# Kernel optimization log

Hardware: AMD Instinct MI355X
Metric: run time of the kernel (lower is better)

## Reference

```python
import jax, jax.numpy as jnp
import numpy as np

B, T, CH, Hs, Ws = 2, 64, 512, 24, 24
DIM = CH // 2          # 256, attention channel dim
HEADS = 8
HEAD_DIM = DIM // HEADS  # 32
MAX_SEQ = 64


def setup_inputs() -> dict:
    key = jax.random.key(0)
    ks = jax.random.split(key, 6)
    return {
        "x": jax.random.normal(ks[0], (B, T, CH, Hs, Ws), dtype=jnp.float32),
        "rpb_table": jax.random.normal(ks[1], (2 * MAX_SEQ - 1, HEADS), dtype=jnp.float32) * 0.02,
        "qkv_w": jax.random.normal(ks[2], (3 * DIM, DIM), dtype=jnp.float32) * 0.02,
        "qkv_b": jax.random.normal(ks[3], (3 * DIM,), dtype=jnp.float32) * 0.02,
        "proj_w": jax.random.normal(ks[4], (DIM, DIM), dtype=jnp.float32) * 0.02,
        "proj_b": jax.random.normal(ks[5], (DIM,), dtype=jnp.float32) * 0.02,
    }


def reference(x, rpb_table, qkv_w, qkv_b, proj_w, proj_b):
    b, t, c, h, w = x.shape
    half = c // 2
    a_part = x[:, :, :half]       # (B,T,half,H,W) untouched branch
    b_part = x[:, :, half:]       # attention branch

    # 'b t c h w -> (b h w) t c'
    xb = jnp.transpose(b_part, (0, 3, 4, 1, 2)).reshape(b * h * w, t, half)
    B_, N, C = xb.shape
    scale = HEAD_DIM ** -0.5

    qkv = xb @ qkv_w.T + qkv_b                        # (B_, N, 3*C)
    qkv = qkv.reshape(B_, N, 3, HEADS, HEAD_DIM)
    qkv = jnp.transpose(qkv, (2, 0, 3, 1, 4))          # (3, B_, heads, N, hd)
    q, k, v = qkv[0] * scale, qkv[1], qkv[2]

    attn = jnp.einsum('bhnd,bhmd->bhnm', q, k)         # (B_, heads, N, N)

    # relative position bias: index = p2 - p1 + (MAX_SEQ - 1)
    pos = jnp.arange(t)
    rel_idx = pos[None, :] - pos[:, None] + (MAX_SEQ - 1)   # (N, N)
    bias = rpb_table[rel_idx]                              # (N, N, heads)
    bias = jnp.transpose(bias, (2, 0, 1))                  # (heads, N, N)
    attn = attn + bias[None]

    # causal (mask_future=True): -inf strictly above the diagonal
    causal = jnp.where(pos[None, :] > pos[:, None], -jnp.inf, 0.0).astype(attn.dtype)
    attn = attn + causal[None, None]

    attn = jax.nn.softmax(attn, axis=-1)

    out = jnp.einsum('bhnm,bhmd->bhnd', attn, v)       # (B_, heads, N, hd)
    out = jnp.transpose(out, (0, 2, 1, 3)).reshape(B_, N, C)
    out = out @ proj_w.T + proj_b

    # '(b h w) t c -> b t c h w'
    out = out.reshape(b, h, w, t, half)
    out = jnp.transpose(out, (0, 3, 4, 1, 2))

    return jnp.concatenate([a_part, out], axis=2)
```

## Files before the change

### kernel.cpp

```cpp
#include <hip/hip_runtime.h>
#include <hip/hip_bf16.h>

typedef __attribute__((ext_vector_type(4))) float  f32x4;
typedef __attribute__((ext_vector_type(8))) short  bf16x8;
typedef __attribute__((ext_vector_type(8))) unsigned short u16x8;

union FU { int w[4]; bf16x8 v; };

__device__ __forceinline__ unsigned short f2bf(float f) {
    union { float f; unsigned u; } v; v.f = f;
    unsigned u = v.u;
    unsigned r = u + 0x7fffu + ((u >> 16) & 1u);
    return (unsigned short)(r >> 16);
}

__device__ __forceinline__ unsigned cvtpk(float lo, float hi) {
    unsigned r;
    asm("v_cvt_pk_bf16_f32 %0, %1, %2" : "=v"(r) : "v"(lo), "v"(hi));
    return r;
}

__device__ __forceinline__ int selshfl(unsigned lo, unsigned hiw, int srcLane, bool hi) {
    int a = __shfl((int)lo, srcLane, 64);
    int b = __shfl((int)hiw, srcLane, 64);
    return hi ? b : a;
}

__device__ __forceinline__ void gload16(const void* g, void* l) {
    __builtin_amdgcn_global_load_lds((const __attribute__((address_space(1))) unsigned*)g,
                                     (__attribute__((address_space(3))) unsigned*)l, 16, 0, 0);
}


__global__ void cvt_weights(const float* __restrict__ qkv_w, const float* __restrict__ proj_w,
                            unsigned short* __restrict__ wq, unsigned short* __restrict__ wp) {
    int i = blockIdx.x * 256 + threadIdx.x;
    if (i < 196608) wq[i] = f2bf(qkv_w[i]);
    else            wp[i - 196608] = f2bf(proj_w[i - 196608]);
}

__global__ __launch_bounds__(256) void transpose_b(const float* __restrict__ x,
                                                   unsigned short* __restrict__ xb,
                                                   float* __restrict__ outp) {
    __shared__ unsigned short tile[256][72];
    const int bt  = blockIdx.x;
    const int hw0 = blockIdx.y * 64;
    const int tid = threadIdx.x;
    {
        const size_t slab = (size_t)bt * 294912;
        #pragma unroll
        for (int it = 0; it < 16; ++it) {
            int idx = it * 256 + tid;
            int ch  = idx >> 4;
            int off = (idx & 15) * 4;
            size_t o = slab + (size_t)ch * 576 + hw0 + off;
            *(float4*)(outp + o) = *(const float4*)(x + o);
        }
    }
    const float* src = x + ((size_t)bt * 512 + 256) * 576 + hw0;
    const int c_sub = tid >> 4, l16 = tid & 15;
    #pragma unroll
    for (int it = 0; it < 16; ++it) {
        int cc = it * 16 + c_sub;
        const float4 v = *(const float4*)(src + (size_t)cc * 576 + l16 * 4);
        tile[cc][l16 * 4 + 0] = f2bf(v.x);
        tile[cc][l16 * 4 + 1] = f2bf(v.y);
        tile[cc][l16 * 4 + 2] = f2bf(v.z);
        tile[cc][l16 * 4 + 3] = f2bf(v.w);
    }
    __syncthreads();
    const int row = tid >> 2;
    const int cs  = (tid & 3) * 64;
    const int b = bt >> 6, t = bt & 63;
    size_t m = ((size_t)(b * 576 + hw0 + row)) * 64 + t;
    unsigned short* dst = xb + m * 256 + cs;
    #pragma unroll
    for (int q = 0; q < 8; ++q) {
        u16x8 v;
        #pragma unroll
        for (int u = 0; u < 8; ++u) v[u] = tile[cs + q * 8 + u][row];
        *(u16x8*)(dst + q * 8) = v;
    }
}

__global__ __launch_bounds__(512, 4)
void fused_block(
    const unsigned short* __restrict__ xb,
    const unsigned short* __restrict__ wqkv,
    const unsigned short* __restrict__ wproj,
    const float* __restrict__ qkv_b,
    const float* __restrict__ proj_b,
    const float* __restrict__ rpb,
    float* __restrict__ out)
{
    __shared__ unsigned short xs[16384];
    __shared__ unsigned short VtAll[256 * 88];
    __shared__ float bias_s[8][64];

    const int tid  = threadIdx.x;
    const int lane = tid & 63, w = tid >> 6;
    const int c = lane & 15, g = lane >> 4;
    const int c7 = c & 7;
    const bool hi = g >= 2;
    const int lA = c + 16 * ((2 * g) & 3);
    const int lB = c + 16 * ((2 * g + 1) & 3);
    const int bid = blockIdx.x;
    const int p  = (bid & 7) * 144 + (bid >> 3);
    const int b  = p / 576, hw = p % 576;

    const unsigned short* src = xb + (size_t)p * 16384;
    #pragma unroll
    for (int it = 0; it < 4; ++it) {
        int U = it * 512 + tid;
        int r = U >> 5, u = U & 31;
        gload16(src + r * 256 + ((u ^ (r & 7)) << 3), &xs[U << 3]);
    }
    bias_s[tid & 7][tid >> 3] = rpb[tid];
    __syncthreads();

    const float* bias_w = bias_s[w];

    {
        f32x4 acc[2][4] = {};
        #pragma unroll
        for (int ks = 0; ks < 8; ++ks) {
            bf16x8 bx[4], af[2];
            #pragma unroll
            for (int b2 = 0; b2 < 4; ++b2)
                bx[b2] = *(const bf16x8*)(&xs[(b2 * 16 + c) * 256 + (((ks * 4 + g) ^ c7) << 3)]);
            #pragma unroll
            for (int a2 = 0; a2 < 2; ++a2)
                af[a2] = *(const bf16x8*)(wqkv + (size_t)(512 + w * 32 + a2 * 16 + c) * 256 + ks * 32 + g * 8);
            #pragma unroll
            for (int a2 = 0; a2 < 2; ++a2)
                #pragma unroll
                for (int b2 = 0; b2 < 4; ++b2)
                    acc[a2][b2] = __builtin_amdgcn_mfma_f32_16x16x32_bf16(af[a2], bx[b2], acc[a2][b2], 0, 0, 0);
        }
        #pragma unroll
        for (int a2 = 0; a2 < 2; ++a2) {
            float4 bv = *(const float4*)(qkv_b + 512 + w * 32 + a2 * 16 + g * 4);
            #pragma unroll
            for (int b2 = 0; b2 < 4; ++b2) {
                int t = b2 * 16 + c;
                VtAll[(w * 32 + a2 * 16 + g * 4 + 0) * 88 + t] = f2bf(acc[a2][b2][0] + bv.x);
                VtAll[(w * 32 + a2 * 16 + g * 4 + 1) * 88 + t] = f2bf(acc[a2][b2][1] + bv.y);
                VtAll[(w * 32 + a2 * 16 + g * 4 + 2) * 88 + t] = f2bf(acc[a2][b2][2] + bv.z);
                VtAll[(w * 32 + a2 * 16 + g * 4 + 3) * 88 + t] = f2bf(acc[a2][b2][3] + bv.w);
            }
        }
    }

    unsigned kpk[2][4][2], qpk[2][4][2];
    {
        f32x4 ak[2][4] = {}, aq[2][4] = {};
        #pragma unroll
        for (int ks = 0; ks < 8; ++ks) {
            bf16x8 bx[4], afk[2], afq[2];
            #pragma unroll
            for (int b2 = 0; b2 < 4; ++b2)
                bx[b2] = *(const bf16x8*)(&xs[(b2 * 16 + c) * 256 + (((ks * 4 + g) ^ c7) << 3)]);
            #pragma unroll
            for (int a2 = 0; a2 < 2; ++a2) {
                afk[a2] = *(const bf16x8*)(wqkv + (size_t)(256 + w * 32 + a2 * 16 + c) * 256 + ks * 32 + g * 8);
                afq[a2] = *(const bf16x8*)(wqkv + (size_t)(      w * 32 + a2 * 16 + c) * 256 + ks * 32 + g * 8);
            }
            #pragma unroll
            for (int a2 = 0; a2 < 2; ++a2)
                #pragma unroll
                for (int b2 = 0; b2 < 4; ++b2) {
                    ak[a2][b2] = __builtin_amdgcn_mfma_f32_16x16x32_bf16(afk[a2], bx[b2], ak[a2][b2], 0, 0, 0);
                    aq[a2][b2] = __builtin_amdgcn_mfma_f32_16x16x32_bf16(afq[a2], bx[b2], aq[a2][b2], 0, 0, 0);
                }
        }
        #pragma unroll
        for (int a2 = 0; a2 < 2; ++a2) {
            float4 bk = *(const float4*)(qkv_b + 256 + w * 32 + a2 * 16 + g * 4);
            float4 bq = *(const float4*)(qkv_b +       w * 32 + a2 * 16 + g * 4);
            #pragma unroll
            for (int b2 = 0; b2 < 4; ++b2) {
                kpk[a2][b2][0] = cvtpk(ak[a2][b2][0] + bk.x, ak[a2][b2][1] + bk.y);
                kpk[a2][b2][1] = cvtpk(ak[a2][b2][2] + bk.z, ak[a2][b2][3] + bk.w);
                qpk[a2][b2][0] = cvtpk(aq[a2][b2][0] + bq.x, aq[a2][b2][1] + bq.y);
                qpk[a2][b2][1] = cvtpk(aq[a2][b2][2] + bq.z, aq[a2][b2][3] + bq.w);
            }
        }
    }

    bf16x8 kf[4], qf[4];
    #pragma unroll
    for (int t = 0; t < 4; ++t) {
        FU f;
        f.w[0] = selshfl(kpk[0][t][0], kpk[1][t][0], lA, hi);
        f.w[1] = selshfl(kpk[0][t][1], kpk[1][t][1], lA, hi);
        f.w[2] = selshfl(kpk[0][t][0], kpk[1][t][0], lB, hi);
        f.w[3] = selshfl(kpk[0][t][1], kpk[1][t][1], lB, hi);
        kf[t] = f.v;
        FU f2;
        f2.w[0] = selshfl(qpk[0][t][0], qpk[1][t][0], lA, hi);
        f2.w[1] = selshfl(qpk[0][t][1], qpk[1][t][1], lA, hi);
        f2.w[2] = selshfl(qpk[0][t][0], qpk[1][t][0], lB, hi);
        f2.w[3] = selshfl(qpk[0][t][1], qpk[1][t][1], lB, hi);
        qf[t] = f2.v;
    }
    f32x4 S[4][4];
    #pragma unroll
    for (int jt = 0; jt < 4; ++jt)
        #pragma unroll
        for (int it = 0; it < 4; ++it)
            S[jt][it] = f32x4{0.f, 0.f, 0.f, 0.f};
    __builtin_amdgcn_s_setprio(1);
    #pragma unroll
    for (int jt = 0; jt < 4; ++jt)
        #pragma unroll
        for (int it = 0; it < 4; ++it)
            S[jt][it] = __builtin_amdgcn_mfma_f32_16x16x32_bf16(kf[jt], qf[it], S[jt][it], 0, 0, 0);
    __builtin_amdgcn_s_setprio(0);

    const float scale = 0.17677669529663687f;
    unsigned ppk[4][4][2];
    #pragma unroll
    for (int it = 0; it < 4; ++it) {
        float rs = 0.f;
        #pragma unroll
        for (int jt = 0; jt < 4; ++jt)
            #pragma unroll
            for (int r = 0; r < 4; ++r) {
                int j = jt * 16 + 4 * g + r;
                int i = it * 16 + c;
                int d = j - i + 63; d = d > 63 ? 63 : d;
                float v = S[jt][it][r] * scale + bias_w[d];
                float e = (j > i) ? 0.f : __expf(v);
                S[jt][it][r] = e;
                rs += e;
            }
        rs += __shfl_xor(rs, 16, 64);
        rs += __shfl_xor(rs, 32, 64);
        float inv = 1.0f / rs;
        #pragma unroll
        for (int jt = 0; jt < 4; ++jt) {
            ppk[jt][it][0] = cvtpk(S[jt][it][0] * inv, S[jt][it][1] * inv);
            ppk[jt][it][1] = cvtpk(S[jt][it][2] * inv, S[jt][it][3] * inv);
        }
    }

    bf16x8 vf[2][2];
    #pragma unroll
    for (int dt = 0; dt < 2; ++dt)
        #pragma unroll
        for (int kk = 0; kk < 2; ++kk)
            vf[dt][kk] = *(const bf16x8*)(&VtAll[(w * 32 + dt * 16 + c) * 88 + kk * 32 + g * 8]);
    f32x4 O[2][4];
    #pragma unroll
    for (int dt = 0; dt < 2; ++dt)
        #pragma unroll
        for (int it = 0; it < 4; ++it)
            O[dt][it] = f32x4{0.f, 0.f, 0.f, 0.f};
    #pragma unroll
    for (int it = 0; it < 4; ++it) {
        #pragma unroll
        for (int kk = 0; kk < 2; ++kk) {
            FU pf;
            pf.w[0] = selshfl(ppk[2 * kk][it][0], ppk[2 * kk + 1][it][0], lA, hi);
            pf.w[1] = selshfl(ppk[2 * kk][it][1], ppk[2 * kk + 1][it][1], lA, hi);
            pf.w[2] = selshfl(ppk[2 * kk][it][0], ppk[2 * kk + 1][it][0], lB, hi);
            pf.w[3] = selshfl(ppk[2 * kk][it][1], ppk[2 * kk + 1][it][1], lB, hi);
            __builtin_amdgcn_s_setprio(1);
            #pragma unroll
            for (int dt = 0; dt < 2; ++dt)
                O[dt][it] = __builtin_amdgcn_mfma_f32_16x16x32_bf16(vf[dt][kk], pf.v, O[dt][it], 0, 0, 0);
            __builtin_amdgcn_s_setprio(0);
        }
    }

    __syncthreads();
    #pragma unroll
    for (int dt = 0; dt < 2; ++dt)
        #pragma unroll
        for (int it = 0; it < 4; ++it)
            #pragma unroll
            for (int r = 0; r < 4; ++r) {
                int t  = it * 16 + c;
                int cg = w * 32 + dt * 16 + 4 * g + r;
                xs[t * 256 + ((((cg >> 3) ^ (t & 7)) << 3) | (cg & 7))] = f2bf(O[dt][it][r]);
            }
    __syncthreads();

    f32x4 ap[2][4] = {};
    #pragma unroll
    for (int ks = 0; ks < 8; ++ks) {
        bf16x8 af[2], bx[4];
        #pragma unroll
        for (int a2 = 0; a2 < 2; ++a2)
            af[a2] = *(const bf16x8*)(wproj + (size_t)(w * 32 + a2 * 16 + c) * 256 + ks * 32 + g * 8);
        #pragma unroll
        for (int b2 = 0; b2 < 4; ++b2)
            bx[b2] = *(const bf16x8*)(&xs[(b2 * 16 + c) * 256 + (((ks * 4 + g) ^ c7) << 3)]);
        #pragma unroll
        for (int a2 = 0; a2 < 2; ++a2)
            #pragma unroll
            for (int b2 = 0; b2 < 4; ++b2)
                ap[a2][b2] = __builtin_amdgcn_mfma_f32_16x16x32_bf16(af[a2], bx[b2], ap[a2][b2], 0, 0, 0);
    }
    #pragma unroll
    for (int a2 = 0; a2 < 2; ++a2) {
        int n = w * 32 + a2 * 16 + g * 4;
        float4 pb = *(const float4*)(proj_b + n);
        #pragma unroll
        for (int b2 = 0; b2 < 4; ++b2) {
            int t = b2 * 16 + c;
            float* dst = out + ((size_t)((b * 64 + t) * 512 + 256 + n)) * 576 + hw;
            dst[0]        = ap[a2][b2][0] + pb.x;
            dst[576]      = ap[a2][b2][1] + pb.y;
            dst[2 * 576]  = ap[a2][b2][2] + pb.z;
            dst[3 * 576]  = ap[a2][b2][3] + pb.w;
        }
    }
}

extern "C" void kernel_launch(void* const* d_in, const int* in_sizes, int n_in,
                              void* d_out, int out_size, void* d_ws, size_t ws_size,
                              hipStream_t stream) {
    (void)in_sizes; (void)n_in; (void)out_size;
    const float* x      = (const float*)d_in[0];
    const float* rpb    = (const float*)d_in[1];
    const float* qkv_w  = (const float*)d_in[2];
    const float* qkv_b  = (const float*)d_in[3];
    const float* proj_w = (const float*)d_in[4];
    const float* proj_b = (const float*)d_in[5];
    float* out = (float*)d_out;

    char* ws = (char*)d_ws;
    unsigned short* wq = (unsigned short*)ws;
    unsigned short* wp = (unsigned short*)(ws + 393216);
    unsigned short* xb = (unsigned short*)(ws + 524288);
    if (ws_size < (size_t)524288 + 37748736) return;

    cvt_weights<<<1024, 256, 0, stream>>>(qkv_w, proj_w, wq, wp);
    transpose_b<<<dim3(128, 9), 256, 0, stream>>>(x, xb, out);
    fused_block<<<1152, 512, 0, stream>>>(xb, wq, wp, qkv_b, proj_b, rpb, out);
}
```

Measured before the change: 250.0 us.

## Process attention per query tile to cut live registers and pin waves per EU

```diff
diff --git a/kernel.cpp b/kernel.cpp
--- a/kernel.cpp
+++ b/kernel.cpp
@@ -83,7 +83,7 @@
     }
 }
 
-__global__ __launch_bounds__(512, 4)
+__global__ __launch_bounds__(512) __attribute__((amdgpu_waves_per_eu(4, 4)))
 void fused_block(
     const unsigned short* __restrict__ xb,
     const unsigned short* __restrict__ wqkv,
@@ -187,7 +187,7 @@
         }
     }
 
-    bf16x8 kf[4], qf[4];
+    bf16x8 kf[4];
     #pragma unroll
     for (int t = 0; t < 4; ++t) {
         FU f;
@@ -196,75 +196,66 @@
         f.w[2] = selshfl(kpk[0][t][0], kpk[1][t][0], lB, hi);
         f.w[3] = selshfl(kpk[0][t][1], kpk[1][t][1], lB, hi);
         kf[t] = f.v;
-        FU f2;
-        f2.w[0] = selshfl(qpk[0][t][0], qpk[1][t][0], lA, hi);
-        f2.w[1] = selshfl(qpk[0][t][1], qpk[1][t][1], lA, hi);
-        f2.w[2] = selshfl(qpk[0][t][0], qpk[1][t][0], lB, hi);
-        f2.w[3] = selshfl(qpk[0][t][1], qpk[1][t][1], lB, hi);
-        qf[t] = f2.v;
-    }
-    f32x4 S[4][4];
-    #pragma unroll
-    for (int jt = 0; jt < 4; ++jt)
+    }
+    bf16x8 vf[2][2];
+    #pragma unroll
+    for (int dt = 0; dt < 2; ++dt)
+        #pragma unroll
+        for (int kk = 0; kk < 2; ++kk)
+            vf[dt][kk] = *(const bf16x8*)(&VtAll[(w * 32 + dt * 16 + c) * 88 + kk * 32 + g * 8]);
+
+    const float scale = 0.17677669529663687f;
+    f32x4 O[2][4];
+    #pragma unroll
+    for (int dt = 0; dt < 2; ++dt)
         #pragma unroll
         for (int it = 0; it < 4; ++it)
-            S[jt][it] = f32x4{0.f, 0.f, 0.f, 0.f};
-    __builtin_amdgcn_s_setprio(1);
-    #pragma unroll
-    for (int jt = 0; jt < 4; ++jt)
-        #pragma unroll
-        for (int it = 0; it < 4; ++it)
-            S[jt][it] = __builtin_amdgcn_mfma_f32_16x16x32_bf16(kf[jt], qf[it], S[jt][it], 0, 0, 0);
-    __builtin_amdgcn_s_setprio(0);
-
-    const float scale = 0.17677669529663687f;
-    unsigned ppk[4][4][2];
+            O[dt][it] = f32x4{0.f, 0.f, 0.f, 0.f};
+
     #pragma unroll
     for (int it = 0; it < 4; ++it) {
+        FU fq;
+        fq.w[0] = selshfl(qpk[0][it][0], qpk[1][it][0], lA, hi);
+        fq.w[1] = selshfl(qpk[0][it][1], qpk[1][it][1], lA, hi);
+        fq.w[2] = selshfl(qpk[0][it][0], qpk[1][it][0], lB, hi);
+        fq.w[3] = selshfl(qpk[0][it][1], qpk[1][it][1], lB, hi);
+        f32x4 Sc[4];
+        #pragma unroll
+        for (int jt = 0; jt < 4; ++jt) Sc[jt] = f32x4{0.f, 0.f, 0.f, 0.f};
+        __builtin_amdgcn_s_setprio(1);
+        #pragma unroll
+        for (int jt = 0; jt < 4; ++jt)
+            Sc[jt] = __builtin_amdgcn_mfma_f32_16x16x32_bf16(kf[jt], fq.v, Sc[jt], 0, 0, 0);
+        __builtin_amdgcn_s_setprio(0);
         float rs = 0.f;
+        const int i = it * 16 + c;
         #pragma unroll
         for (int jt = 0; jt < 4; ++jt)
             #pragma unroll
             for (int r = 0; r < 4; ++r) {
                 int j = jt * 16 + 4 * g + r;
-                int i = it * 16 + c;
                 int d = j - i + 63; d = d > 63 ? 63 : d;
-                float v = S[jt][it][r] * scale + bias_w[d];
+                float v = Sc[jt][r] * scale + bias_w[d];
                 float e = (j > i) ? 0.f : __expf(v);
-                S[jt][it][r] = e;
+                Sc[jt][r] = e;
                 rs += e;
             }
         rs += __shfl_xor(rs, 16, 64);
         rs += __shfl_xor(rs, 32, 64);
         float inv = 1.0f / rs;
+        unsigned pc[4][2];
         #pragma unroll
         for (int jt = 0; jt < 4; ++jt) {
-            ppk[jt][it][0] = cvtpk(S[jt][it][0] * inv, S[jt][it][1] * inv);
-            ppk[jt][it][1] = cvtpk(S[jt][it][2] * inv, S[jt][it][3] * inv);
-        }
-    }
-
-    bf16x8 vf[2][2];
-    #pragma unroll
-    for (int dt = 0; dt < 2; ++dt)
-        #pragma unroll
-        for (int kk = 0; kk < 2; ++kk)
-            vf[dt][kk] = *(const bf16x8*)(&VtAll[(w * 32 + dt * 16 + c) * 88 + kk * 32 + g * 8]);
-    f32x4 O[2][4];
-    #pragma unroll
-    for (int dt = 0; dt < 2; ++dt)
-        #pragma unroll
-        for (int it = 0; it < 4; ++it)
-            O[dt][it] = f32x4{0.f, 0.f, 0.f, 0.f};
-    #pragma unroll
-    for (int it = 0; it < 4; ++it) {
+            pc[jt][0] = cvtpk(Sc[jt][0] * inv, Sc[jt][1] * inv);
+            pc[jt][1] = cvtpk(Sc[jt][2] * inv, Sc[jt][3] * inv);
+        }
         #pragma unroll
         for (int kk = 0; kk < 2; ++kk) {
             FU pf;
-            pf.w[0] = selshfl(ppk[2 * kk][it][0], ppk[2 * kk + 1][it][0], lA, hi);
-            pf.w[1] = selshfl(ppk[2 * kk][it][1], ppk[2 * kk + 1][it][1], lA, hi);
-            pf.w[2] = selshfl(ppk[2 * kk][it][0], ppk[2 * kk + 1][it][0], lB, hi);
-            pf.w[3] = selshfl(ppk[2 * kk][it][1], ppk[2 * kk + 1][it][1], lB, hi);
+            pf.w[0] = selshfl(pc[2 * kk][0], pc[2 * kk + 1][0], lA, hi);
+            pf.w[1] = selshfl(pc[2 * kk][1], pc[2 * kk + 1][1], lA, hi);
+            pf.w[2] = selshfl(pc[2 * kk][0], pc[2 * kk + 1][0], lB, hi);
+            pf.w[3] = selshfl(pc[2 * kk][1], pc[2 * kk + 1][1], lB, hi);
             __builtin_amdgcn_s_setprio(1);
             #pragma unroll
             for (int dt = 0; dt < 2; ++dt)
```

Measured after the change: 251.8 us. About the same (+0.7%).
